# Performance work log

Measured on AMD Instinct MI355X. Metric: run time of the kernel, lower is better.

## Reference

```python
import jax, jax.numpy as jnp
import jax.lax as lax
import numpy as np

X_NUM = 512
Y_NUM = 512
GRID = 1.0 / 512.0
MIN_X = 0.0
MIN_Y = 0.0
N_POINTS = 400000
BATCH = 4
NUM_CLASSES = 20


def setup_inputs():
    key = jax.random.key(0)
    ks = jax.random.split(key, 32)
    # rows 0/1: x,y coords in [0,1) so they land inside the 512x512 grid; rows 2-5: features
    xy = jax.random.uniform(ks[0], (2, N_POINTS), jnp.float32, 0.0, 1.0 - 1e-6)
    feat = jax.random.normal(ks[1], (4, N_POINTS), jnp.float32) * 0.5
    points = jnp.concatenate([xy, feat], 0)
    batch_ids = jax.random.randint(ks[2], (N_POINTS,), 0, BATCH, jnp.int32)
    inp = {"batch_ids": batch_ids, "points": points, "batch_size": BATCH}

    def lin(k, o, i):
        return jax.random.normal(k, (o, i), jnp.float32) * (1.0 / np.sqrt(i))

    ki = 3
    # pointwise conv1d stacks: (name, out_ch, in_ch)
    for name, o, i in [("0", 16, 6), ("1", 16, 16), ("v0", 16, 18), ("v1", 16, 32), ("2", 32, 32)]:
        inp["w" + name] = lin(ks[ki], o, i); ki += 1
        inp["b" + name] = jnp.zeros((o,), jnp.float32)
        inp["s" + name] = jax.random.uniform(ks[ki], (o,), jnp.float32, 0.5, 1.5); ki += 1
        inp["t" + name] = jax.random.normal(ks[ki], (o,), jnp.float32) * 0.1; ki += 1
    inp["w2d"] = jax.random.normal(ks[ki], (4, 32, 32, 3, 3), jnp.float32) * (1.0 / np.sqrt(32 * 9)); ki += 1
    inp["b2d"] = jnp.zeros((4, 32), jnp.float32)
    inp["s2d"] = jax.random.uniform(ks[ki], (4, 32), jnp.float32, 0.5, 1.5); ki += 1
    inp["t2d"] = jax.random.normal(ks[ki], (4, 32), jnp.float32) * 0.1; ki += 1
    inp["w3"] = lin(ks[ki], NUM_CLASSES, 64); ki += 1
    inp["b3"] = jnp.zeros((NUM_CLASSES,), jnp.float32)
    return inp


def _pconv(x, w, b, s, t):
    # 1x1 conv1d + BatchNorm(inference affine) + ReLU; x: [Cin, N]
    return jax.nn.relu((w @ x + b[:, None]) * s[:, None] + t[:, None])


def _scatter_max(v, gids, n):
    # v: [C, N] -> [C, n]; empty segments filled with 0 (torch_scatter fill_value=0,
    # and all scattered values here are post-ReLU >= 0)
    seg = jax.ops.segment_max(v.T, gids, num_segments=n).T
    return jnp.where(jnp.isneginf(seg), 0.0, seg)


def _bilinear(img, ix, iy):
    # grid_sample(align_corners=False, padding zeros) in pixel coords; img: [C, H, W]
    C, H, W = img.shape
    x0 = jnp.floor(ix); y0 = jnp.floor(iy)
    wx = ix - x0; wy = iy - y0
    x0i = x0.astype(jnp.int32); y0i = y0.astype(jnp.int32)

    def tap(yi, xi):
        valid = ((yi >= 0) & (yi < H) & (xi >= 0) & (xi < W)).astype(img.dtype)
        return img[:, jnp.clip(yi, 0, H - 1), jnp.clip(xi, 0, W - 1)] * valid

    return (tap(y0i, x0i) * (1 - wx) * (1 - wy) + tap(y0i, x0i + 1) * wx * (1 - wy)
            + tap(y0i + 1, x0i) * (1 - wx) * wy + tap(y0i + 1, x0i + 1) * wx * wy)


def _forward(batch_ids, points, batch_size, w0, b0, s0, t0, w1, b1, s1, t1,
             wv0, bv0, sv0, tv0, wv1, bv1, sv1, tv1, w2, b2, s2, t2,
             w2d, b2d, s2d, t2d, w3, b3):
    x_g = jnp.floor((points[0] - MIN_X) / GRID).astype(jnp.int32)
    y_g = jnp.floor((points[1] - MIN_Y) / GRID).astype(jnp.int32)
    gids = batch_ids.astype(jnp.int32) * (X_NUM * Y_NUM) + y_g * X_NUM + x_g
    grid_num = batch_size * Y_NUM * X_NUM

    h = _pconv(points, w0, b0, s0, t0)       # [16, N]
    h = _pconv(h, w1, b1, s1, t1)            # [16, N]
    vx = (x_g.astype(jnp.float32) + 0.5) * GRID + MIN_X
    vy = (y_g.astype(jnp.float32) + 0.5) * GRID + MIN_Y
    h = jnp.concatenate([h, (points[0] - vx)[None], (points[1] - vy)[None]], 0)  # [18, N]

    # VFE blocks: pointwise conv -> scatter_max over voxel ids -> gather back -> concat
    o = _pconv(h, wv0, bv0, sv0, tv0)        # [16, N]
    h = jnp.concatenate([o, _scatter_max(o, gids, grid_num)[:, gids]], 0)  # [32, N]
    o = _pconv(h, wv1, bv1, sv1, tv1)        # [16, N]
    h = jnp.concatenate([o, _scatter_max(o, gids, grid_num)[:, gids]], 0)  # [32, N]

    point0 = _pconv(h, w2, b2, s2, t2)       # [32, N]
    grid = _scatter_max(point0, gids, grid_num)
    grid = grid.reshape(32, batch_size, Y_NUM, X_NUM).transpose(1, 0, 2, 3)  # [B,32,Y,X]

    for i in range(4):
        p = 1 if i == 0 else 2
        grid = lax.conv_general_dilated(grid, w2d[i], (1, 1), ((p, p), (p, p)),
                                        rhs_dilation=(p, p),
                                        dimension_numbers=("NCHW", "OIHW", "NCHW"))
        grid = jax.nn.relu((grid + b2d[i][None, :, None, None]) * s2d[i][None, :, None, None]
                           + t2d[i][None, :, None, None])

    # interpolate (grid_sample) back to points; pixel coords reduce to (x-MIN)/GRID - 1
    img = grid.transpose(1, 0, 2, 3).reshape(32, batch_size * Y_NUM, X_NUM)
    ix = (points[0] - MIN_X) / GRID - 1.0
    iy = (points[1] - MIN_Y) / GRID - 1.0 + batch_ids.astype(jnp.float32) * Y_NUM
    point1 = _bilinear(img, ix, iy)          # [32, N]

    point = jnp.concatenate([point0, point1], 0)  # [64, N]
    return w3 @ point + b3[:, None]               # [num_classes, N]


def reference(batch_ids, points, batch_size, w0, b0, s0, t0, w1, b1, s1, t1,
              wv0, bv0, sv0, tv0, wv1, bv1, sv1, tv1, w2, b2, s2, t2,
              w2d, b2d, s2d, t2d, w3, b3):
    return _forward(batch_ids, points, batch_size, w0, b0, s0, t0, w1, b1, s1, t1,
                    wv0, bv0, sv0, tv0, wv1, bv1, sv1, tv1, w2, b2, s2, t2,
                    w2d, b2d, s2d, t2d, w3, b3)
```

## Files before the change

kernel.cpp:

```cpp
#include <hip/hip_runtime.h>
#include <hip/hip_bf16.h>
#include <hip/hip_fp16.h>

#define N_PTS 400000
#define XN 512
#define YN 512
#define BATCHN 4
#define VOX (XN*YN)
#define GRID_NUM (BATCHN*VOX)

typedef unsigned long long u64;
typedef __attribute__((ext_vector_type(8))) _Float16 f16x8;
typedef __attribute__((ext_vector_type(4))) float f32x4;

static __device__ __forceinline__ float relu_(float x){ return fmaxf(x, 0.0f); }
static __device__ __forceinline__ int voxel_id(float px, float py, int b){
    int xg = (int)floorf(px*512.0f);
    int yg = (int)floorf(py*512.0f);
    return b*VOX + yg*XN + xg;
}

static __device__ __forceinline__ u64 packh4(const float* v){
    u64 r = 0;
    #pragma unroll
    for (int j=0;j<4;j++){
        unsigned short h = __half_as_ushort(__float2half_rn(v[j]));
        r |= (u64)h << (16*j);
    }
    return r;
}
static __device__ __forceinline__ void unpackh4(u64 w, float* o){
    #pragma unroll
    for (int j=0;j<4;j++)
        o[j] = __half2float(__ushort_as_half((unsigned short)(w >> (16*j))));
}
static __device__ __forceinline__ u64 pkmax4(u64 a, u64 b){
    u64 r = 0;
    #pragma unroll
    for (int j=0;j<4;j++){
        u64 x = (a >> (16*j)) & 0xFFFFull;
        u64 y = (b >> (16*j)) & 0xFFFFull;
        r |= (x > y ? x : y) << (16*j);
    }
    return r;
}

__global__ void kZero(float4* __restrict__ p, int n4){
    int i = blockIdx.x*256 + threadIdx.x;
    const float4 z = make_float4(0.f,0.f,0.f,0.f);
    for (; i < n4; i += gridDim.x*256) p[i] = z;
}

__global__ void kDiag(float* __restrict__ o, int n, float v){
    int i = blockIdx.x*256 + threadIdx.x;
    for (; i < n; i += gridDim.x*256) o[i] = v;
}

__global__ void kWprep(const float* __restrict__ W32, _Float16* __restrict__ wf){
    int idx = blockIdx.x*256 + threadIdx.x;
    if (idx >= 4*9216) return;
    int L = idx / 9216, r = idx % 9216;
    int j = r & 7, ln = (r>>3) & 63, rest = r >> 9;
    int t = rest >> 1, nt = rest & 1;
    int ic = (ln>>4)*8 + j, oc = nt*16 + (ln&15);
    wf[idx] = (_Float16)W32[(size_t)L*9216 + ((size_t)oc*32 + ic)*9 + t];
}

__global__ void kHist(const int* __restrict__ bid, const float* __restrict__ pts,
                      unsigned* __restrict__ offs, int* __restrict__ gids)
{
    int i = blockIdx.x*256 + threadIdx.x;
    if (i >= N_PTS) return;
    int gid = voxel_id(pts[i], pts[N_PTS+i], bid[i]);
    gids[i] = gid;
    atomicAdd(&offs[gid], 1u);
}

__global__ void kScan1(unsigned* __restrict__ offs, unsigned* __restrict__ partials)
{
    __shared__ unsigned sa[256], sb[256];
    const int t = threadIdx.x;
    const int g = blockIdx.x*256 + t;
    unsigned v = offs[g];
    sa[t] = v;
    __syncthreads();
    unsigned* src = sa; unsigned* dst = sb;
    #pragma unroll
    for (int d=1; d<256; d<<=1){
        dst[t] = src[t] + ((t>=d) ? src[t-d] : 0u);
        __syncthreads();
        unsigned* tmp = src; src = dst; dst = tmp;
    }
    unsigned incl = src[t];
    offs[g] = incl - v;
    if (t == 255) partials[blockIdx.x] = incl;
}
__global__ void kScan2(unsigned* __restrict__ partials)
{
    __shared__ unsigned sa[256], sb[256];
    const int t = threadIdx.x;
    unsigned loc[16]; unsigned sum = 0;
    #pragma unroll
    for (int j=0;j<16;j++){ loc[j] = partials[t*16+j]; sum += loc[j]; }
    sa[t] = sum;
    __syncthreads();
    unsigned* src = sa; unsigned* dst = sb;
    #pragma unroll
    for (int d=1; d<256; d<<=1){
        dst[t] = src[t] + ((t>=d) ? src[t-d] : 0u);
        __syncthreads();
        unsigned* tmp = src; src = dst; dst = tmp;
    }
    unsigned run = src[t] - sum;
    #pragma unroll
    for (int j=0;j<16;j++){ unsigned c = loc[j]; partials[t*16+j] = run; run += c; }
}
__global__ void kScan3(unsigned* __restrict__ offs, const unsigned* __restrict__ partials)
{
    int g = blockIdx.x*256 + threadIdx.x;
    offs[g] += partials[blockIdx.x];
}

__global__ void kA(const int* __restrict__ bid, const float* __restrict__ pts,
                   const int* __restrict__ gids,
                   const float* __restrict__ w0, const float* __restrict__ b0,
                   const float* __restrict__ s0, const float* __restrict__ t0,
                   const float* __restrict__ w1, const float* __restrict__ b1,
                   const float* __restrict__ s1, const float* __restrict__ t1,
                   const float* __restrict__ wv0, const float* __restrict__ bv0,
                   const float* __restrict__ sv0, const float* __restrict__ tv0,
                   u64* __restrict__ obufA,
                   unsigned* __restrict__ offs, unsigned* __restrict__ order)
{
    int i = blockIdx.x*256 + threadIdx.x;
    if (i >= N_PTS) return;
    float p[6];
    #pragma unroll
    for (int r=0;r<6;r++) p[r] = pts[r*N_PTS+i];
    int xg = (int)floorf(p[0]*512.0f);
    int yg = (int)floorf(p[1]*512.0f);

    float h0[16];
    #pragma unroll
    for (int o=0;o<16;o++){
        float a = b0[o];
        #pragma unroll
        for (int k=0;k<6;k++) a = fmaf(w0[o*6+k], p[k], a);
        h0[o] = relu_(fmaf(a, s0[o], t0[o]));
    }
    float h1[16];
    #pragma unroll
    for (int o=0;o<16;o++){
        float a = b1[o];
        #pragma unroll
        for (int k=0;k<16;k++) a = fmaf(w1[o*16+k], h0[k], a);
        h1[o] = relu_(fmaf(a, s1[o], t1[o]));
    }
    float dx = p[0] - ((float)xg + 0.5f)*(1.0f/512.0f);
    float dy = p[1] - ((float)yg + 0.5f)*(1.0f/512.0f);
    float vv[16];
    #pragma unroll
    for (int o=0;o<16;o++){
        float a = bv0[o];
        #pragma unroll
        for (int k=0;k<16;k++) a = fmaf(wv0[o*18+k], h1[k], a);
        a = fmaf(wv0[o*18+16], dx, a);
        a = fmaf(wv0[o*18+17], dy, a);
        vv[o] = relu_(fmaf(a, sv0[o], tv0[o]));
    }
    u64* op = obufA + (size_t)i*4;
    #pragma unroll
    for (int q=0;q<4;q++) op[q] = packh4(&vv[q*4]);

    int gid = gids[i];
    unsigned pos = atomicAdd(&offs[gid], 1u);
    order[pos] = (unsigned)i;
}

__global__ void kSegMax(const unsigned* __restrict__ offs, const unsigned* __restrict__ order,
                        const u64* __restrict__ src, u64* __restrict__ dst)
{
    int v = blockIdx.x*256 + threadIdx.x;
    unsigned s = v ? offs[v-1] : 0u;
    unsigned e = offs[v];
    if (e <= s) return;
    u64 m0=0,m1=0,m2=0,m3=0;
    for (unsigned p=s; p<e; ++p){
        const u64* q = src + (size_t)order[p]*4;
        m0 = pkmax4(m0, q[0]); m1 = pkmax4(m1, q[1]);
        m2 = pkmax4(m2, q[2]); m3 = pkmax4(m3, q[3]);
    }
    u64* d = dst + (size_t)v*4;
    d[0]=m0; d[1]=m1; d[2]=m2; d[3]=m3;
}

__global__ void kGridMax(const unsigned* __restrict__ offs, const unsigned* __restrict__ order,
                         const u64* __restrict__ src, u64* __restrict__ dst)
{
    int v = blockIdx.x*256 + threadIdx.x;
    unsigned s = v ? offs[v-1] : 0u;
    unsigned e = offs[v];
    u64 m[8];
    #pragma unroll
    for (int q=0;q<8;q++) m[q] = 0ull;
    for (unsigned p=s; p<e; ++p){
        const u64* q = src + (size_t)order[p]*8;
        #pragma unroll
        for (int j=0;j<8;j++) m[j] = pkmax4(m[j], q[j]);
    }
    u64* d = dst + (size_t)v*8;
    #pragma unroll
    for (int q=0;q<8;q++) d[q] = m[q];
}

__global__ void kB(const int* __restrict__ gids,
                   const float* __restrict__ w, const float* __restrict__ bb,
                   const float* __restrict__ ss, const float* __restrict__ tt,
                   const u64* __restrict__ obufA, const u64* __restrict__ seg0,
                   u64* __restrict__ obufB)
{
    int i = blockIdx.x*256 + threadIdx.x;
    if (i >= N_PTS) return;
    int gid = gids[i];
    float h[32];
    const u64* ap = obufA + (size_t)i*4;
    #pragma unroll
    for (int q=0;q<4;q++) unpackh4(ap[q], &h[q*4]);
    const u64* sp = seg0 + (size_t)gid*4;
    #pragma unroll
    for (int q=0;q<4;q++) unpackh4(sp[q], &h[16+q*4]);

    float o[16];
    #pragma unroll
    for (int c=0;c<16;c++){
        float a = bb[c];
        #pragma unroll
        for (int k=0;k<32;k++) a = fmaf(w[c*32+k], h[k], a);
        o[c] = relu_(fmaf(a, ss[c], tt[c]));
    }
    u64* op = obufB + (size_t)i*4;
    #pragma unroll
    for (int q=0;q<4;q++) op[q] = packh4(&o[q*4]);
}

__global__ void kC(const int* __restrict__ gids,
                   const float* __restrict__ w, const float* __restrict__ bb,
                   const float* __restrict__ ss, const float* __restrict__ tt,
                   const float* __restrict__ w3,
                   const u64* __restrict__ obufB, const u64* __restrict__ seg1,
                   u64* __restrict__ pbuf, float* __restrict__ outp)
{
    int i = blockIdx.x*256 + threadIdx.x;
    if (i >= N_PTS) return;
    int gid = gids[i];
    float h[32];
    const u64* ap = obufB + (size_t)i*4;
    #pragma unroll
    for (int q=0;q<4;q++) unpackh4(ap[q], &h[q*4]);
    const u64* sp = seg1 + (size_t)gid*4;
    #pragma unroll
    for (int q=0;q<4;q++) unpackh4(sp[q], &h[16+q*4]);

    float p0v[32];
    #pragma unroll
    for (int c=0;c<32;c++){
        float a = bb[c];
        #pragma unroll
        for (int k=0;k<32;k++) a = fmaf(w[c*32+k], h[k], a);
        p0v[c] = relu_(fmaf(a, ss[c], tt[c]));
    }
    u64* pp = pbuf + (size_t)i*8;
    #pragma unroll
    for (int q=0;q<8;q++) pp[q] = packh4(&p0v[q*4]);
    #pragma unroll
    for (int k=0;k<20;k++){
        float a = 0.f;
        #pragma unroll
        for (int c=0;c<32;c++) a = fmaf(w3[k*64+c], p0v[c], a);
        outp[(size_t)k*N_PTS+i] = a;
    }
}

template<int P>
__global__ __launch_bounds__(256,4) void convM(
    const _Float16* __restrict__ in, _Float16* __restrict__ out,
    const f16x8* __restrict__ wfrag, const float* __restrict__ bb,
    const float* __restrict__ ss, const float* __restrict__ tt)
{
    constexpr int TW = 32, TH = 8;
    constexpr int TIW = TW + 2*P, TIH = TH + 2*P;
    __shared__ uint4 sA[TIH*TIW*5];
    const int tid = threadIdx.x;
    const int lane = tid & 63, wv = tid >> 6;
    const int x0 = blockIdx.x*TW, y0 = blockIdx.y*TH, bz = blockIdx.z;
    const _Float16* inB = in + (size_t)bz*VOX*32;

    for (int u = tid; u < TIH*TIW*4; u += 256){
        int g = u & 3;
        int pxr = u >> 2;
        int px = pxr % TIW, r = pxr / TIW;
        int gy = y0 - P + r, gx = x0 - P + px;
        uint4 v = make_uint4(0,0,0,0);
        if ((unsigned)gy < 512u && (unsigned)gx < 512u)
            v = *(const uint4*)(inB + (((size_t)gy*512 + gx)*32 + g*8));
        sA[(r*TIW + px)*5 + g] = v;
    }
    __syncthreads();

    const f16x8* pA = (const f16x8*)sA;
    const int aoff = (lane&15)*5 + (lane>>4);
    const int rowbase = wv*2;

    f32x4 acc[4][2];
    #pragma unroll
    for (int m=0;m<4;m++){ acc[m][0]=(f32x4)0.f; acc[m][1]=(f32x4)0.f; }

    #pragma unroll
    for (int t=0;t<9;t++){
        const int ky = t/3, kx = t%3;
        f16x8 b0 = wfrag[(t*2+0)*64 + lane];
        f16x8 b1 = wfrag[(t*2+1)*64 + lane];
        #pragma unroll
        for (int m=0;m<4;m++){
            int r = rowbase + (m>>1) + ky*P;
            int pxb = (m&1)*16 + kx*P;
            f16x8 a = pA[(r*TIW + pxb)*5 + aoff];
            acc[m][0] = __builtin_amdgcn_mfma_f32_16x16x32_f16(b0, a, acc[m][0], 0,0,0);
            acc[m][1] = __builtin_amdgcn_mfma_f32_16x16x32_f16(b1, a, acc[m][1], 0,0,0);
        }
    }

    float bn[2][4], sn[2][4], tn[2][4];
    #pragma unroll
    for (int n=0;n<2;n++){
        int ocb = n*16 + (lane>>4)*4;
        #pragma unroll
        for (int r=0;r<4;r++){ bn[n][r]=bb[ocb+r]; sn[n][r]=ss[ocb+r]; tn[n][r]=tt[ocb+r]; }
    }
    _Float16* outB = out + (size_t)bz*VOX*32;
    #pragma unroll
    for (int m=0;m<4;m++){
        int y  = y0 + rowbase + (m>>1);
        int px = x0 + (m&1)*16 + (lane&15);
        #pragma unroll
        for (int n=0;n<2;n++){
            unsigned h[4];
            #pragma unroll
            for (int r=0;r<4;r++){
                float v = relu_(fmaf(acc[m][n][r] + bn[n][r], sn[n][r], tn[n][r]));
                h[r] = (unsigned)__half_as_ushort(__float2half_rn(v));
            }
            uint2 val = make_uint2(h[0] | (h[1]<<16), h[2] | (h[3]<<16));
            *(uint2*)(outB + ((size_t)y*512 + px)*32 + n*16 + (lane>>4)*4) = val;
        }
    }
}

__global__ void kFinal(const int* __restrict__ bid, const float* __restrict__ pts,
                       const _Float16* __restrict__ gridH,
                       const float* __restrict__ w3, const float* __restrict__ b3,
                       float* __restrict__ outp)
{
    int i = blockIdx.x*256 + threadIdx.x;
    if (i >= N_PTS) return;
    float px = pts[i], py = pts[N_PTS+i];
    int b = bid[i];
    float ix = px*512.0f - 1.0f;
    float iy = py*512.0f - 1.0f + (float)(b*512);
    float x0f = floorf(ix), y0f = floorf(iy);
    float wx = ix - x0f, wy = iy - y0f;
    int x0 = (int)x0f, y0 = (int)y0f;

    float p1[32];
    #pragma unroll
    for (int c=0;c<32;c++) p1[c] = 0.f;
    #pragma unroll
    for (int t=0;t<4;t++){
        int yi = y0 + (t>>1);
        int xi = x0 + (t&1);
        if (yi < 0 || yi >= BATCHN*YN || xi < 0 || xi >= XN) continue;
        float wgt = ((t>>1)? wy : 1.0f-wy) * ((t&1)? wx : 1.0f-wx);
        const uint4* tp = (const uint4*)(gridH + ((size_t)yi*XN + xi)*32);
        #pragma unroll
        for (int q=0;q<4;q++){
            uint4 v = tp[q];
            const unsigned int* vu = (const unsigned int*)&v;
            #pragma unroll
            for (int e=0;e<4;e++){
                float lo = __half2float(__ushort_as_half((unsigned short)(vu[e] & 0xFFFF)));
                float hi = __half2float(__ushort_as_half((unsigned short)(vu[e] >> 16)));
                p1[q*8 + e*2 + 0] = fmaf(wgt, lo, p1[q*8 + e*2 + 0]);
                p1[q*8 + e*2 + 1] = fmaf(wgt, hi, p1[q*8 + e*2 + 1]);
            }
        }
    }

    #pragma unroll
    for (int k=0;k<20;k++){
        float a = outp[(size_t)k*N_PTS + i] + b3[k];
        #pragma unroll
        for (int c=0;c<32;c++) a = fmaf(w3[k*64+32+c], p1[c], a);
        outp[(size_t)k*N_PTS + i] = a;
    }
}

extern "C" void kernel_launch(void* const* d_in, const int* in_sizes, int n_in,
                              void* d_out, int out_size, void* d_ws, size_t ws_size,
                              hipStream_t stream)
{
    const int*   bid = (const int*)  d_in[0];
    const float* pts = (const float*)d_in[1];
    const float* w0  = (const float*)d_in[3];
    const float* b0  = (const float*)d_in[4];
    const float* s0  = (const float*)d_in[5];
    const float* t0  = (const float*)d_in[6];
    const float* w1  = (const float*)d_in[7];
    const float* b1  = (const float*)d_in[8];
    const float* s1  = (const float*)d_in[9];
    const float* t1  = (const float*)d_in[10];
    const float* wv0 = (const float*)d_in[11];
    const float* bv0 = (const float*)d_in[12];
    const float* sv0 = (const float*)d_in[13];
    const float* tv0 = (const float*)d_in[14];
    const float* wv1 = (const float*)d_in[15];
    const float* bv1 = (const float*)d_in[16];
    const float* sv1 = (const float*)d_in[17];
    const float* tv1 = (const float*)d_in[18];
    const float* w2  = (const float*)d_in[19];
    const float* b2  = (const float*)d_in[20];
    const float* s2  = (const float*)d_in[21];
    const float* t2  = (const float*)d_in[22];
    const float* w2d = (const float*)d_in[23];
    const float* b2d = (const float*)d_in[24];
    const float* s2d = (const float*)d_in[25];
    const float* t2d = (const float*)d_in[26];
    const float* w3  = (const float*)d_in[27];
    const float* b3  = (const float*)d_in[28];

    const size_t MB = 1024*1024;
    const size_t NEED = 192*MB;
    if (ws_size < NEED){
        kDiag<<<512,256,0,stream>>>((float*)d_out, out_size, (float)(ws_size>>20));
        return;
    }

    char* ws = (char*)d_ws;
    u64*      gridV    = (u64*)ws;
    _Float16* ping     = (_Float16*)ws;
    _Float16* pong     = (_Float16*)(ws + 64*MB);
    u64*      seg0     = (u64*)(ws + 64*MB);
    u64*      seg1     = (u64*)(ws + 96*MB);
    unsigned* offs     = (unsigned*)(ws + 128*MB);
    unsigned* partials = (unsigned*)(ws + 132*MB);
    unsigned* order    = (unsigned*)(ws + 133*MB);
    int*      gids     = (int*)(ws + 135*MB);
    u64*      obufA    = (u64*)(ws + 137*MB);
    u64*      obufB    = (u64*)(ws + 150*MB);
    u64*      pbuf     = (u64*)(ws + 163*MB);
    _Float16* wfrag    = (_Float16*)(ws + 189*MB);

    kZero<<<256,256,0,stream>>>((float4*)offs, (int)(GRID_NUM*4/16));
    kWprep<<<144,256,0,stream>>>(w2d, wfrag);

    const int nb = (N_PTS + 255)/256;
    const int nv = GRID_NUM/256;

    kHist <<<nb,256,0,stream>>>(bid, pts, offs, gids);
    kScan1<<<nv,256,0,stream>>>(offs, partials);
    kScan2<<<1,256,0,stream>>>(partials);
    kScan3<<<nv,256,0,stream>>>(offs, partials);

    kA<<<nb,256,0,stream>>>(bid, pts, gids, w0,b0,s0,t0, w1,b1,s1,t1,
                            wv0,bv0,sv0,tv0, obufA, offs, order);
    kSegMax<<<nv,256,0,stream>>>(offs, order, obufA, seg0);
    kB<<<nb,256,0,stream>>>(gids, wv1,bv1,sv1,tv1, obufA, seg0, obufB);
    kSegMax<<<nv,256,0,stream>>>(offs, order, obufB, seg1);
    kC<<<nb,256,0,stream>>>(gids, w2,b2,s2,t2, w3, obufB, seg1, pbuf, (float*)d_out);
    kGridMax<<<nv,256,0,stream>>>(offs, order, pbuf, gridV);

    dim3 cgrid(XN/32, YN/8, BATCHN);
    const f16x8* wf = (const f16x8*)wfrag;
    convM<1><<<cgrid,256,0,stream>>>(ping, pong, wf + 0*1152, b2d + 0,  s2d + 0,  t2d + 0);
    convM<2><<<cgrid,256,0,stream>>>(pong, ping, wf + 1*1152, b2d + 32, s2d + 32, t2d + 32);
    convM<2><<<cgrid,256,0,stream>>>(ping, pong, wf + 2*1152, b2d + 64, s2d + 64, t2d + 64);
    convM<2><<<cgrid,256,0,stream>>>(pong, ping, wf + 3*1152, b2d + 96, s2d + 96, t2d + 96);

    kFinal<<<nb,256,0,stream>>>(bid, pts, ping, w3, b3, (float*)d_out);
}
```

Baseline: 356.7 us.

## Store per-point features in voxel-sorted order to make segment max reads contiguous

Point features are now written at their sorted (voxel-grouped) slot in kA instead of by point index, together with a sorted gid array and an inverse permutation. Segment-max and grid-max kernels then read contiguous rows without going through the order indirection, and kB/kC run in sorted order so their seg lookups are coherent. The first half of the final linear layer moves from kC to kFinal, which gathers pbuf through the inverse permutation. This avoids a read-modify-write of the output, at the cost of one scattered gather per point in kFinal.

```diff
diff --git a/kernel.cpp b/kernel.cpp
--- a/kernel.cpp
+++ b/kernel.cpp
@@ -129,8 +129,8 @@
                    const float* __restrict__ s1, const float* __restrict__ t1,
                    const float* __restrict__ wv0, const float* __restrict__ bv0,
                    const float* __restrict__ sv0, const float* __restrict__ tv0,
-                   u64* __restrict__ obufA,
-                   unsigned* __restrict__ offs, unsigned* __restrict__ order)
+                   u64* __restrict__ obufA, unsigned* __restrict__ offs,
+                   int* __restrict__ sGid, unsigned* __restrict__ inv)
 {
     int i = blockIdx.x*256 + threadIdx.x;
     if (i >= N_PTS) return;
@@ -168,16 +168,16 @@
         a = fmaf(wv0[o*18+17], dy, a);
         vv[o] = relu_(fmaf(a, sv0[o], tv0[o]));
     }
-    u64* op = obufA + (size_t)i*4;
-    #pragma unroll
-    for (int q=0;q<4;q++) op[q] = packh4(&vv[q*4]);
-
     int gid = gids[i];
     unsigned pos = atomicAdd(&offs[gid], 1u);
-    order[pos] = (unsigned)i;
-}
-
-__global__ void kSegMax(const unsigned* __restrict__ offs, const unsigned* __restrict__ order,
+    u64* op = obufA + (size_t)pos*4;
+    #pragma unroll
+    for (int q=0;q<4;q++) op[q] = packh4(&vv[q*4]);
+    sGid[pos] = gid;
+    inv[i] = pos;
+}
+
+__global__ void kSegMax(const unsigned* __restrict__ offs,
                         const u64* __restrict__ src, u64* __restrict__ dst)
 {
     int v = blockIdx.x*256 + threadIdx.x;
@@ -186,7 +186,7 @@
     if (e <= s) return;
     u64 m0=0,m1=0,m2=0,m3=0;
     for (unsigned p=s; p<e; ++p){
-        const u64* q = src + (size_t)order[p]*4;
+        const u64* q = src + (size_t)p*4;
         m0 = pkmax4(m0, q[0]); m1 = pkmax4(m1, q[1]);
         m2 = pkmax4(m2, q[2]); m3 = pkmax4(m3, q[3]);
     }
@@ -194,7 +194,7 @@
     d[0]=m0; d[1]=m1; d[2]=m2; d[3]=m3;
 }
 
-__global__ void kGridMax(const unsigned* __restrict__ offs, const unsigned* __restrict__ order,
+__global__ void kGridMax(const unsigned* __restrict__ offs,
                          const u64* __restrict__ src, u64* __restrict__ dst)
 {
     int v = blockIdx.x*256 + threadIdx.x;
@@ -204,7 +204,7 @@
     #pragma unroll
     for (int q=0;q<8;q++) m[q] = 0ull;
     for (unsigned p=s; p<e; ++p){
-        const u64* q = src + (size_t)order[p]*8;
+        const u64* q = src + (size_t)p*8;
         #pragma unroll
         for (int j=0;j<8;j++) m[j] = pkmax4(m[j], q[j]);
     }
@@ -213,17 +213,17 @@
     for (int q=0;q<8;q++) d[q] = m[q];
 }
 
-__global__ void kB(const int* __restrict__ gids,
+__global__ void kB(const int* __restrict__ sGid,
                    const float* __restrict__ w, const float* __restrict__ bb,
                    const float* __restrict__ ss, const float* __restrict__ tt,
                    const u64* __restrict__ obufA, const u64* __restrict__ seg0,
                    u64* __restrict__ obufB)
 {
-    int i = blockIdx.x*256 + threadIdx.x;
-    if (i >= N_PTS) return;
-    int gid = gids[i];
+    int j = blockIdx.x*256 + threadIdx.x;
+    if (j >= N_PTS) return;
+    int gid = sGid[j];
     float h[32];
-    const u64* ap = obufA + (size_t)i*4;
+    const u64* ap = obufA + (size_t)j*4;
     #pragma unroll
     for (int q=0;q<4;q++) unpackh4(ap[q], &h[q*4]);
     const u64* sp = seg0 + (size_t)gid*4;
@@ -238,23 +238,22 @@
         for (int k=0;k<32;k++) a = fmaf(w[c*32+k], h[k], a);
         o[c] = relu_(fmaf(a, ss[c], tt[c]));
     }
-    u64* op = obufB + (size_t)i*4;
+    u64* op = obufB + (size_t)j*4;
     #pragma unroll
     for (int q=0;q<4;q++) op[q] = packh4(&o[q*4]);
 }
 
-__global__ void kC(const int* __restrict__ gids,
+__global__ void kC(const int* __restrict__ sGid,
                    const float* __restrict__ w, const float* __restrict__ bb,
                    const float* __restrict__ ss, const float* __restrict__ tt,
-                   const float* __restrict__ w3,
                    const u64* __restrict__ obufB, const u64* __restrict__ seg1,
-                   u64* __restrict__ pbuf, float* __restrict__ outp)
-{
-    int i = blockIdx.x*256 + threadIdx.x;
-    if (i >= N_PTS) return;
-    int gid = gids[i];
+                   u64* __restrict__ pbuf)
+{
+    int j = blockIdx.x*256 + threadIdx.x;
+    if (j >= N_PTS) return;
+    int gid = sGid[j];
     float h[32];
-    const u64* ap = obufB + (size_t)i*4;
+    const u64* ap = obufB + (size_t)j*4;
     #pragma unroll
     for (int q=0;q<4;q++) unpackh4(ap[q], &h[q*4]);
     const u64* sp = seg1 + (size_t)gid*4;
@@ -269,16 +268,9 @@
         for (int k=0;k<32;k++) a = fmaf(w[c*32+k], h[k], a);
         p0v[c] = relu_(fmaf(a, ss[c], tt[c]));
     }
-    u64* pp = pbuf + (size_t)i*8;
+    u64* pp = pbuf + (size_t)j*8;
     #pragma unroll
     for (int q=0;q<8;q++) pp[q] = packh4(&p0v[q*4]);
-    #pragma unroll
-    for (int k=0;k<20;k++){
-        float a = 0.f;
-        #pragma unroll
-        for (int c=0;c<32;c++) a = fmaf(w3[k*64+c], p0v[c], a);
-        outp[(size_t)k*N_PTS+i] = a;
-    }
 }
 
 template<int P>
@@ -357,6 +349,7 @@
 }
 
 __global__ void kFinal(const int* __restrict__ bid, const float* __restrict__ pts,
+                       const unsigned* __restrict__ inv, const u64* __restrict__ pbuf,
                        const _Float16* __restrict__ gridH,
                        const float* __restrict__ w3, const float* __restrict__ b3,
                        float* __restrict__ outp)
@@ -365,6 +358,12 @@
     if (i >= N_PTS) return;
     float px = pts[i], py = pts[N_PTS+i];
     int b = bid[i];
+
+    float p0[32];
+    const u64* pp = pbuf + (size_t)inv[i]*8;
+    #pragma unroll
+    for (int q=0;q<8;q++) unpackh4(pp[q], &p0[q*4]);
+
     float ix = px*512.0f - 1.0f;
     float iy = py*512.0f - 1.0f + (float)(b*512);
     float x0f = floorf(ix), y0f = floorf(iy);
@@ -397,7 +396,9 @@
 
     #pragma unroll
     for (int k=0;k<20;k++){
-        float a = outp[(size_t)k*N_PTS + i] + b3[k];
+        float a = b3[k];
+        #pragma unroll
+        for (int c=0;c<32;c++) a = fmaf(w3[k*64+c], p0[c], a);
         #pragma unroll
         for (int c=0;c<32;c++) a = fmaf(w3[k*64+32+c], p1[c], a);
         outp[(size_t)k*N_PTS + i] = a;
@@ -452,12 +453,13 @@
     u64*      seg1     = (u64*)(ws + 96*MB);
     unsigned* offs     = (unsigned*)(ws + 128*MB);
     unsigned* partials = (unsigned*)(ws + 132*MB);
-    unsigned* order    = (unsigned*)(ws + 133*MB);
+    int*      sGid     = (int*)(ws + 133*MB);
     int*      gids     = (int*)(ws + 135*MB);
-    u64*      obufA    = (u64*)(ws + 137*MB);
-    u64*      obufB    = (u64*)(ws + 150*MB);
-    u64*      pbuf     = (u64*)(ws + 163*MB);
-    _Float16* wfrag    = (_Float16*)(ws + 189*MB);
+    unsigned* inv      = (unsigned*)(ws + 137*MB);
+    u64*      obufA    = (u64*)(ws + 139*MB);
+    u64*      obufB    = (u64*)(ws + 152*MB);
+    u64*      pbuf     = (u64*)(ws + 165*MB);
+    _Float16* wfrag    = (_Float16*)(ws + 191*MB);
 
     kZero<<<256,256,0,stream>>>((float4*)offs, (int)(GRID_NUM*4/16));
     kWprep<<<144,256,0,stream>>>(w2d, wfrag);
@@ -471,12 +473,12 @@
     kScan3<<<nv,256,0,stream>>>(offs, partials);
 
     kA<<<nb,256,0,stream>>>(bid, pts, gids, w0,b0,s0,t0, w1,b1,s1,t1,
-                            wv0,bv0,sv0,tv0, obufA, offs, order);
-    kSegMax<<<nv,256,0,stream>>>(offs, order, obufA, seg0);
-    kB<<<nb,256,0,stream>>>(gids, wv1,bv1,sv1,tv1, obufA, seg0, obufB);
-    kSegMax<<<nv,256,0,stream>>>(offs, order, obufB, seg1);
-    kC<<<nb,256,0,stream>>>(gids, w2,b2,s2,t2, w3, obufB, seg1, pbuf, (float*)d_out);
-    kGridMax<<<nv,256,0,stream>>>(offs, order, pbuf, gridV);
+                            wv0,bv0,sv0,tv0, obufA, offs, sGid, inv);
+    kSegMax<<<nv,256,0,stream>>>(offs, obufA, seg0);
+    kB<<<nb,256,0,stream>>>(sGid, wv1,bv1,sv1,tv1, obufA, seg0, obufB);
+    kSegMax<<<nv,256,0,stream>>>(offs, obufB, seg1);
+    kC<<<nb,256,0,stream>>>(sGid, w2,b2,s2,t2, obufB, seg1, pbuf);
+    kGridMax<<<nv,256,0,stream>>>(offs, pbuf, gridV);
 
     dim3 cgrid(XN/32, YN/8, BATCHN);
     const f16x8* wf = (const f16x8*)wfrag;
@@ -485,5 +487,5 @@
     convM<2><<<cgrid,256,0,stream>>>(ping, pong, wf + 2*1152, b2d + 64, s2d + 64, t2d + 64);
     convM<2><<<cgrid,256,0,stream>>>(pong, ping, wf + 3*1152, b2d + 96, s2d + 96, t2d + 96);
 
-    kFinal<<<nb,256,0,stream>>>(bid, pts, ping, w3, b3, (float*)d_out);
-}
+    kFinal<<<nb,256,0,stream>>>(bid, pts, inv, pbuf, ping, w3, b3, (float*)d_out);
+}
```

After: 344.1 us. -3.5%, faster.
